# Optimization experiments

Measured on AMD Instinct MI355X. Metric: run time of the kernel, lower is better.

Reference implementation:

```python
import jax, jax.numpy as jnp
import numpy as np

H, W = 4096, 4096
KH, KW = 11, 11


def setup_inputs() -> dict:
    key = jax.random.key(0)
    k1, k2 = jax.random.split(key)
    x = jax.random.normal(k1, (H, W), dtype=jnp.float32)
    weight = jax.random.uniform(k2, (KH, KW), dtype=jnp.float32)
    bias = jnp.zeros((1,), dtype=jnp.float32)
    return {"x": x, "weight": weight, "bias": bias}


def reference(x, weight, bias):
    # corr2d: valid 2D cross-correlation of a single-channel image with a
    # single kernel, then add scalar bias. Output shape [H-KH+1, W-KW+1].
    out = jax.lax.conv_general_dilated(
        x[None, None, :, :],            # NCHW, N=C=1
        weight[None, None, :, :],       # OIHW, O=I=1
        window_strides=(1, 1),
        padding="VALID",
        dimension_numbers=("NCHW", "OIHW", "NCHW"),
    )[0, 0]
    return out + bias[0]
```

## Files before the change

### kernel.cpp

```cpp
#include <hip/hip_runtime.h>
#include <hip/hip_bf16.h>

#define IH 4096
#define IW 4096
#define KH 11
#define KW 11
#define OH (IH - KH + 1)
#define OW (IW - KW + 1)

#define BM 64
#define BN 64
#define TROWS   74
#define TSTRIDE 84
#define NC4     20
#define NCHUNK  (TROWS * NC4)
#define NITER   6
#define TILE_SHORTS (TROWS * TSTRIDE)

#define TILES_X 64
#define NBLK    1024

typedef short bf16x4 __attribute__((ext_vector_type(4)));
typedef short bf16x8 __attribute__((ext_vector_type(8)));
typedef float f32x4  __attribute__((ext_vector_type(4)));

__device__ __forceinline__ short f2b(float f) {
    __hip_bfloat16 h = __float2bfloat16(f);
    return __builtin_bit_cast(short, h);
}

__device__ __forceinline__ void stage_load(float4 G[NITER],
                                           const float* __restrict__ x,
                                           int gx0, int gy0, int tid) {
#pragma unroll
    for (int it = 0; it < NITER; ++it) {
        const int i = tid + it * 256;
        float4 v = make_float4(0.f, 0.f, 0.f, 0.f);
        if (i < NCHUNK) {
            const int r  = i / NC4;
            const int c4 = i - r * NC4;
            const int gy = gy0 + r;
            const int gx = gx0 + c4 * 4;
            if (gy < IH && gx + 3 < IW) {
                v = *reinterpret_cast<const float4*>(x + (size_t)gy * IW + gx);
            }
        }
        G[it] = v;
    }
}

__device__ __forceinline__ void stage_write(short* __restrict__ tb,
                                            const float4 G[NITER], int tid) {
#pragma unroll
    for (int it = 0; it < NITER; ++it) {
        const int i = tid + it * 256;
        if (i < NCHUNK) {
            const int r  = i / NC4;
            const int c4 = i - r * NC4;
            bf16x4 b = { f2b(G[it].x), f2b(G[it].y), f2b(G[it].z), f2b(G[it].w) };
            *reinterpret_cast<bf16x4*>(&tb[r * TSTRIDE + c4 * 4]) = b;
        }
    }
}

__device__ __forceinline__ void loadA(bf16x8 a[4], const short* __restrict__ ap) {
#pragma unroll
    for (int c = 0; c < 4; ++c) {
        bf16x4 lo = *reinterpret_cast<const bf16x4*>(ap + c * 16);
        bf16x4 hi = *reinterpret_cast<const bf16x4*>(ap + c * 16 + 4);
        a[c] = __builtin_shufflevector(lo, hi, 0, 1, 2, 3, 4, 5, 6, 7);
    }
}

__device__ __forceinline__ void mfma4(f32x4 acc[4], const bf16x8 a[4], bf16x8 b) {
#pragma unroll
    for (int c = 0; c < 4; ++c) {
        acc[c] = __builtin_amdgcn_mfma_f32_16x16x32_bf16(a[c], b, acc[c], 0, 0, 0);
    }
}

__device__ __forceinline__ void compute_tile(const short* __restrict__ tb,
                                             const short* __restrict__ bmat,
                                             float bv, float* __restrict__ out,
                                             int gx0, int gy0,
                                             int wv, int g, int li) {
    f32x4 acc[4] = {};
    const short* ap = &tb[(16 * wv + li) * TSTRIDE + g * 8];
    const short* bp = &bmat[li * 32 + g * 8];

    bf16x8 Ae[4], Ao[4], Be, Bo;
    loadA(Ae, ap);
    Be = *reinterpret_cast<const bf16x8*>(bp);

#pragma unroll 1
    for (int kh2 = 0; kh2 < 5; ++kh2) {
        loadA(Ao, ap + TSTRIDE);
        Bo = *reinterpret_cast<const bf16x8*>(bp + 512);
        mfma4(acc, Ae, Be);
        ap += 2 * TSTRIDE;
        bp += 1024;
        loadA(Ae, ap);
        Be = *reinterpret_cast<const bf16x8*>(bp);
        mfma4(acc, Ao, Bo);
    }
    mfma4(acc, Ae, Be);

#pragma unroll
    for (int c = 0; c < 4; ++c) {
        const int ox = gx0 + c * 16 + li;
        if (ox < OW) {
#pragma unroll
            for (int r = 0; r < 4; ++r) {
                const int oy = gy0 + wv * 16 + g * 4 + r;
                if (oy < OH) {
                    out[(size_t)oy * OW + ox] = acc[c][r] + bv;
                }
            }
        }
    }
}

__global__ __launch_bounds__(256)
void conv2d_mfma5(const float* __restrict__ x,
                  const float* __restrict__ w,
                  const float* __restrict__ bias,
                  float* __restrict__ out) {
    __shared__ short buf[2][TILE_SHORTS];
    __shared__ short bmat[KH * 512];

    const int tid = threadIdx.x;
    const int blk = (blockIdx.x & 7) * (NBLK / 8) + (blockIdx.x >> 3);
    const int t0  = blk * 4;
    const int gy0 = (t0 >> 6) * BM;
    const int gxb = (t0 & (TILES_X - 1)) * BN;

    const int lane = tid & 63;
    const int wv   = tid >> 6;
    const int g    = lane >> 4;
    const int li   = lane & 15;
    const float bv = bias[0];

    {
        float4 G0[NITER];
        stage_load(G0, x, gxb, gy0, tid);
        stage_write(buf[0], G0, tid);
    }
#pragma unroll
    for (int t = 0; t < 22; ++t) {
        const int idx = tid + t * 256;
        const int kh = idx >> 9;
        const int j  = (idx >> 5) & 15;
        const int k  = idx & 31;
        const int d  = k - j;
        const float val = (d >= 0 && d < KW) ? w[kh * KW + d] : 0.f;
        bmat[idx] = f2b(val);
    }
    __syncthreads();

    float4 G[NITER];
#pragma unroll 1
    for (int t = 0; t < 4; ++t) {
        if (t < 3) {
            stage_load(G, x, gxb + (t + 1) * BN, gy0, tid);
            __builtin_amdgcn_sched_barrier(0);
        }
        compute_tile(buf[t & 1], bmat, bv, out, gxb + t * BN, gy0, wv, g, li);
        if (t < 3) {
            stage_write(buf[(t + 1) & 1], G, tid);
            __syncthreads();
        }
    }
}

extern "C" void kernel_launch(void* const* d_in, const int* in_sizes, int n_in,
                              void* d_out, int out_size, void* d_ws, size_t ws_size,
                              hipStream_t stream) {
    const float* x    = (const float*)d_in[0];
    const float* w    = (const float*)d_in[1];
    const float* bias = (const float*)d_in[2];
    float* out        = (float*)d_out;

    dim3 grid(NBLK);
    dim3 block(256);
    conv2d_mfma5<<<grid, block, 0, stream>>>(x, w, bias, out);
}
```

Measured before the change: 38.33 us.

## Precompute banded weight matrix in separate kernel and halve tiles per block

The banded Toeplitz bf16 weight matrix is now built once by a tiny pre-kernel into workspace, so blocks no longer rebuild it in shared memory. The main kernel reads B fragments straight from global memory (L2/L1 cached). The grid doubles to 2048 blocks of two tiles each, giving more parallelism and shorter per-block pipelines. The cost is an extra kernel launch, global B loads inside the MFMA loop in place of LDS reads, and less reuse of the prologue across tiles.

```diff
diff --git a/kernel.cpp b/kernel.cpp
--- a/kernel.cpp
+++ b/kernel.cpp
@@ -18,7 +18,8 @@
 #define TILE_SHORTS (TROWS * TSTRIDE)
 
 #define TILES_X 64
-#define NBLK    1024
+#define NPAIR   2048
+#define BMAT_SHORTS (KH * 512)
 
 typedef short bf16x4 __attribute__((ext_vector_type(4)));
 typedef short bf16x8 __attribute__((ext_vector_type(8)));
@@ -27,6 +28,20 @@
 __device__ __forceinline__ short f2b(float f) {
     __hip_bfloat16 h = __float2bfloat16(f);
     return __builtin_bit_cast(short, h);
+}
+
+__global__ void build_bmat(const float* __restrict__ w, short* __restrict__ bm) {
+    const int tid = threadIdx.x;
+#pragma unroll
+    for (int t = 0; t < 22; ++t) {
+        const int idx = tid + t * 256;
+        const int kh = idx >> 9;
+        const int j  = (idx >> 5) & 15;
+        const int k  = idx & 31;
+        const int d  = k - j;
+        const float val = (d >= 0 && d < KW) ? w[kh * KW + d] : 0.f;
+        bm[idx] = f2b(val);
+    }
 }
 
 __device__ __forceinline__ void stage_load(float4 G[NITER],
@@ -80,13 +95,13 @@
 }
 
 __device__ __forceinline__ void compute_tile(const short* __restrict__ tb,
-                                             const short* __restrict__ bmat,
+                                             const short* __restrict__ bg,
                                              float bv, float* __restrict__ out,
                                              int gx0, int gy0,
                                              int wv, int g, int li) {
     f32x4 acc[4] = {};
     const short* ap = &tb[(16 * wv + li) * TSTRIDE + g * 8];
-    const short* bp = &bmat[li * 32 + g * 8];
+    const short* bp = &bg[li * 32 + g * 8];
 
     bf16x8 Ae[4], Ao[4], Be, Bo;
     loadA(Ae, ap);
@@ -121,18 +136,17 @@
 }
 
 __global__ __launch_bounds__(256)
-void conv2d_mfma5(const float* __restrict__ x,
-                  const float* __restrict__ w,
-                  const float* __restrict__ bias,
-                  float* __restrict__ out) {
+void conv2d_g(const float* __restrict__ x,
+              const short* __restrict__ bg,
+              const float* __restrict__ bias,
+              float* __restrict__ out) {
     __shared__ short buf[2][TILE_SHORTS];
-    __shared__ short bmat[KH * 512];
 
     const int tid = threadIdx.x;
-    const int blk = (blockIdx.x & 7) * (NBLK / 8) + (blockIdx.x >> 3);
-    const int t0  = blk * 4;
-    const int gy0 = (t0 >> 6) * BM;
-    const int gxb = (t0 & (TILES_X - 1)) * BN;
+    const int pair = (blockIdx.x & 7) * (NPAIR / 8) + (blockIdx.x >> 3);
+    const int t0   = pair * 2;
+    const int gy0  = (t0 >> 6) * BM;
+    const int gxb  = (t0 & (TILES_X - 1)) * BN;
 
     const int lane = tid & 63;
     const int wv   = tid >> 6;
@@ -145,31 +159,18 @@
         stage_load(G0, x, gxb, gy0, tid);
         stage_write(buf[0], G0, tid);
     }
-#pragma unroll
-    for (int t = 0; t < 22; ++t) {
-        const int idx = tid + t * 256;
-        const int kh = idx >> 9;
-        const int j  = (idx >> 5) & 15;
-        const int k  = idx & 31;
-        const int d  = k - j;
-        const float val = (d >= 0 && d < KW) ? w[kh * KW + d] : 0.f;
-        bmat[idx] = f2b(val);
-    }
     __syncthreads();
 
     float4 G[NITER];
-#pragma unroll 1
-    for (int t = 0; t < 4; ++t) {
-        if (t < 3) {
-            stage_load(G, x, gxb + (t + 1) * BN, gy0, tid);
-            __builtin_amdgcn_sched_barrier(0);
-        }
-        compute_tile(buf[t & 1], bmat, bv, out, gxb + t * BN, gy0, wv, g, li);
-        if (t < 3) {
-            stage_write(buf[(t + 1) & 1], G, tid);
-            __syncthreads();
-        }
-    }
+    stage_load(G, x, gxb + BN, gy0, tid);
+    __builtin_amdgcn_sched_barrier(0);
+
+    compute_tile(buf[0], bg, bv, out, gxb, gy0, wv, g, li);
+
+    stage_write(buf[1], G, tid);
+    __syncthreads();
+
+    compute_tile(buf[1], bg, bv, out, gxb + BN, gy0, wv, g, li);
 }
 
 extern "C" void kernel_launch(void* const* d_in, const int* in_sizes, int n_in,
@@ -179,8 +180,11 @@
     const float* w    = (const float*)d_in[1];
     const float* bias = (const float*)d_in[2];
     float* out        = (float*)d_out;
+    short* bm         = (short*)d_ws;
 
-    dim3 grid(NBLK);
+    build_bmat<<<dim3(1), dim3(256), 0, stream>>>(w, bm);
+
+    dim3 grid(NPAIR);
     dim3 block(256);
-    conv2d_mfma5<<<grid, block, 0, stream>>>(x, w, bias, out);
+    conv2d_g<<<grid, block, 0, stream>>>(x, bm, bias, out);
 }
```

Measured after the change: 43.88 us. 14.5% more time.
